# Performance work log

Hardware: AMD Instinct MI355X
Metric: run time of the kernel (lower is better)

Reference implementation:

```python
import jax, jax.numpy as jnp
import numpy as np

# Production-scale detection head dims
B_TOTAL = 16      # num_tbins(4) * batch_size(4)
NUM_ANCHORS = 100000
NUM_CLASSES = 8


def setup_inputs() -> dict:
    key = jax.random.key(0)
    k1, k2, k3, k4 = jax.random.split(key, 4)
    # anchors [A,4] = (cx, cy, w, h); widths/heights strictly positive
    ctr = jax.random.uniform(k1, (NUM_ANCHORS, 2), jnp.float32) * 512.0
    wh = jax.random.uniform(k2, (NUM_ANCHORS, 2), jnp.float32) * 64.0 + 8.0
    anchors = jnp.concatenate([ctr, wh], axis=-1)
    loc_preds = jax.random.normal(k3, (B_TOTAL, NUM_ANCHORS, 4), jnp.float32)
    # class scores in [0,1] (post-sigmoid semantics)
    cls_preds = jax.nn.sigmoid(jax.random.normal(k4, (B_TOTAL, NUM_ANCHORS, NUM_CLASSES), jnp.float32))
    return {
        "anchors": anchors,
        "loc_preds": loc_preds,
        "cls_preds": cls_preds,
        "varx": 0.1,
        "vary": 0.2,
        "score_thresh": 0.7,
        "batch_size": 4,
    }


def reference(anchors, loc_preds, cls_preds, varx, vary, score_thresh, batch_size):
    """Anchor decode + score-threshold filtering.

    Faithful to BoxDecoder.forward, but jit-compatible: instead of
    boolean-mask compaction into ragged per-(t,i) lists (data-dependent
    shapes), we return the dense [B*A*C, 6] box tensor plus the keep mask
    and batch_index; (mask, batch_index) fully determine the ragged
    targets[t][i] = box_tensor[mask & (batch_index == t*batch_size+i)].
    """
    B, A, C = cls_preds.shape
    # decode: xy = loc[:2]*varx*anchor_wh + anchor_xy ; wh = exp(loc[2:]*vary)*anchor_wh
    xy = loc_preds[..., :2] * varx * anchors[..., 2:] + anchors[..., :2]
    wh = jnp.exp(loc_preds[..., 2:] * vary) * anchors[..., 2:]
    box_preds = jnp.concatenate([xy - wh * 0.5, xy + wh * 0.5], axis=-1)  # [B,A,4]
    # expand boxes over classes, flatten to [B*A*C, ...] (same order as torch view(-1,...))
    boxes = jnp.broadcast_to(box_preds[:, :, None, :], (B, A, C, 4)).reshape(-1, 4)
    scores = cls_preds.reshape(-1)
    # idxs = b*C + c  ->  label = c+1, batch_index = b
    labels = jnp.broadcast_to(jnp.arange(C, dtype=jnp.float32) + 1.0, (B, A, C)).reshape(-1)
    batch_index = jnp.broadcast_to(jnp.arange(B, dtype=jnp.int32)[:, None, None], (B, A, C)).reshape(-1)
    box_tensor = jnp.concatenate([boxes, scores[:, None], labels[:, None]], axis=1)  # [B*A*C, 6]
    mask = scores >= score_thresh  # keep mask (compaction left to consumer / kernel)
    return box_tensor, mask, batch_index
```

## Files before the change

kernel.cpp:

```cpp
#include <hip/hip_runtime.h>
#include <math.h>


#define MAGIC_SHIFT 38

__global__ __launch_bounds__(256) void box_decode_kernel(
    const float4* __restrict__ anchors,
    const float4* __restrict__ loc,
    const float*  __restrict__ cls,
    const float*  __restrict__ varx_p,
    const float*  __restrict__ vary_p,
    const float*  __restrict__ th_p,
    float2*       __restrict__ out_box2,
    float*        __restrict__ out_mask,
    float*        __restrict__ out_bidx,
    unsigned n2,
    unsigned A, unsigned C,
    unsigned long long invA,
    unsigned long long invC)
{
    unsigned j = blockIdx.x * 256u + threadIdx.x;
    if (j >= n2) return;

    unsigned row = j / 3u;
    unsigned rem = j - row * 3u;

    unsigned t = (unsigned)(((unsigned long long)row * invC) >> MAGIC_SHIFT);
    unsigned c = row - t * C;
    unsigned b = (unsigned)(((unsigned long long)t * invA) >> MAGIC_SHIFT);
    unsigned a = t - b * A;

    float varx = *varx_p;
    float vary = *vary_p;
    float th   = *th_p;

    float4 anc = anchors[a];
    float4 lp  = loc[t];

    float x = fmaf(lp.x * varx, anc.z, anc.x);
    float y = fmaf(lp.y * varx, anc.w, anc.y);
    float w = expf(lp.z * vary) * anc.z;
    float h = expf(lp.w * vary) * anc.w;

    float score = cls[row];

    float2 r;
    if (rem == 0) {
        r.x = fmaf(w, -0.5f, x);
        r.y = fmaf(h, -0.5f, y);
    } else if (rem == 1) {
        r.x = fmaf(w, 0.5f, x);
        r.y = fmaf(h, 0.5f, y);
    } else {
        r.x = score;
        r.y = (float)(c + 1u);
    }
    out_box2[j] = r;

    if (rem == 2) {
        out_mask[row] = (score >= th) ? 1.0f : 0.0f;
        out_bidx[row] = (float)b;
    }
}

extern "C" void kernel_launch(void* const* d_in, const int* in_sizes, int n_in,
                              void* d_out, int out_size, void* d_ws, size_t ws_size,
                              hipStream_t stream) {
    const float* anchors = (const float*)d_in[0];
    const float* loc     = (const float*)d_in[1];
    const float* cls     = (const float*)d_in[2];
    const float* varx_p  = (const float*)d_in[3];
    const float* vary_p  = (const float*)d_in[4];
    const float* th_p    = (const float*)d_in[5];

    unsigned A = (unsigned)(in_sizes[0] / 4);
    unsigned B = (unsigned)((unsigned)in_sizes[1] / (4u * A));
    unsigned C = (unsigned)((unsigned)in_sizes[2] / (A * B));
    unsigned rows = B * A * C;
    unsigned n2 = rows * 3u;

    float* out_box  = (float*)d_out;
    float* out_mask = out_box + (size_t)rows * 6;
    float* out_bidx = out_mask + rows;

    unsigned long long invA = ((1ULL << MAGIC_SHIFT) / A) + 1ULL;
    unsigned long long invC = ((1ULL << MAGIC_SHIFT) / C) + 1ULL;

    dim3 grid((n2 + 255u) / 256u);
    box_decode_kernel<<<grid, dim3(256), 0, stream>>>(
        (const float4*)anchors, (const float4*)loc, cls,
        varx_p, vary_p, th_p,
        (float2*)out_box, out_mask, out_bidx,
        n2, A, C, invA, invC);
}
```

Baseline: 551.3 us.

## Widen box stores to float4 and split mask/bidx into separate blocks

Each thread now writes one float4 of the box tensor, with the 6-float rows grouped in pairs of classes so that three float4 stores cover two rows. The mask and batch-index outputs move to a dedicated tail range of blocks that read scores as float4 and write float4 results. This replaces the float2 stores and the scattered scalar mask/bidx writes from one thread in three, cutting store instructions and improving coalescing. In exchange the kernel assumes C is even and rows is divisible by 4, and each box thread still recomputes the exp-based decode.

```diff
diff --git a/kernel.cpp b/kernel.cpp
--- a/kernel.cpp
+++ b/kernel.cpp
@@ -11,55 +11,84 @@
     const float*  __restrict__ varx_p,
     const float*  __restrict__ vary_p,
     const float*  __restrict__ th_p,
-    float2*       __restrict__ out_box2,
-    float*        __restrict__ out_mask,
-    float*        __restrict__ out_bidx,
-    unsigned n2,
+    float4*       __restrict__ out_box4,
+    float4*       __restrict__ out_mask4,
+    float4*       __restrict__ out_bidx4,
+    unsigned n4,
+    unsigned nm4,
+    unsigned nb_box,
     unsigned A, unsigned C,
+    unsigned f4_per_t,
     unsigned long long invA,
-    unsigned long long invC)
+    unsigned long long invC,
+    unsigned long long invF)
 {
-    unsigned j = blockIdx.x * 256u + threadIdx.x;
-    if (j >= n2) return;
+    unsigned tid = threadIdx.x;
 
-    unsigned row = j / 3u;
-    unsigned rem = j - row * 3u;
+    if (blockIdx.x < nb_box) {
+        unsigned g = blockIdx.x * 256u + tid;
+        if (g >= n4) return;
 
-    unsigned t = (unsigned)(((unsigned long long)row * invC) >> MAGIC_SHIFT);
-    unsigned c = row - t * C;
-    unsigned b = (unsigned)(((unsigned long long)t * invA) >> MAGIC_SHIFT);
-    unsigned a = t - b * A;
+        unsigned t  = (unsigned)(((unsigned long long)g * invF) >> MAGIC_SHIFT);
+        unsigned j  = g - t * f4_per_t;
+        unsigned b  = (unsigned)(((unsigned long long)t * invA) >> MAGIC_SHIFT);
+        unsigned a  = t - b * A;
+        unsigned s  = j / 3u;
+        unsigned jm = j - s * 3u;
 
-    float varx = *varx_p;
-    float vary = *vary_p;
-    float th   = *th_p;
+        float varx = *varx_p;
+        float vary = *vary_p;
 
-    float4 anc = anchors[a];
-    float4 lp  = loc[t];
+        float4 anc = anchors[a];
+        float4 lp  = loc[t];
 
-    float x = fmaf(lp.x * varx, anc.z, anc.x);
-    float y = fmaf(lp.y * varx, anc.w, anc.y);
-    float w = expf(lp.z * vary) * anc.z;
-    float h = expf(lp.w * vary) * anc.w;
+        float x = fmaf(lp.x * varx, anc.z, anc.x);
+        float y = fmaf(lp.y * varx, anc.w, anc.y);
+        float w = expf(lp.z * vary) * anc.z;
+        float h = expf(lp.w * vary) * anc.w;
 
-    float score = cls[row];
+        float x1 = fmaf(w, -0.5f, x);
+        float y1 = fmaf(h, -0.5f, y);
+        float x2 = fmaf(w,  0.5f, x);
+        float y2 = fmaf(h,  0.5f, y);
 
-    float2 r;
-    if (rem == 0) {
-        r.x = fmaf(w, -0.5f, x);
-        r.y = fmaf(h, -0.5f, y);
-    } else if (rem == 1) {
-        r.x = fmaf(w, 0.5f, x);
-        r.y = fmaf(h, 0.5f, y);
+        unsigned r0 = t * C + 2u * s;
+
+        float4 r;
+        if (jm == 0u) {
+            r.x = x1; r.y = y1; r.z = x2; r.w = y2;
+        } else if (jm == 1u) {
+            r.x = cls[r0];
+            r.y = (float)(2u * s + 1u);
+            r.z = x1; r.w = y1;
+        } else {
+            r.x = x2; r.y = y2;
+            r.z = cls[r0 + 1u];
+            r.w = (float)(2u * s + 2u);
+        }
+        out_box4[g] = r;
     } else {
-        r.x = score;
-        r.y = (float)(c + 1u);
-    }
-    out_box2[j] = r;
+        unsigned k = (blockIdx.x - nb_box) * 256u + tid;
+        if (k >= nm4) return;
 
-    if (rem == 2) {
-        out_mask[row] = (score >= th) ? 1.0f : 0.0f;
-        out_bidx[row] = (float)b;
+        float th = *th_p;
+        const float4* cls4 = (const float4*)cls;
+        float4 sc = cls4[k];
+
+        unsigned row0 = k * 4u;
+        unsigned t2 = (unsigned)(((unsigned long long)row0 * invC) >> MAGIC_SHIFT);
+        unsigned b  = (unsigned)(((unsigned long long)t2  * invA) >> MAGIC_SHIFT);
+        float bf = (float)b;
+
+        float4 m;
+        m.x = (sc.x >= th) ? 1.0f : 0.0f;
+        m.y = (sc.y >= th) ? 1.0f : 0.0f;
+        m.z = (sc.z >= th) ? 1.0f : 0.0f;
+        m.w = (sc.w >= th) ? 1.0f : 0.0f;
+        out_mask4[k] = m;
+
+        float4 bv; bv.x = bf; bv.y = bf; bv.z = bf; bv.w = bf;
+        out_bidx4[k] = bv;
     }
 }
 
@@ -77,7 +106,10 @@
     unsigned B = (unsigned)((unsigned)in_sizes[1] / (4u * A));
     unsigned C = (unsigned)((unsigned)in_sizes[2] / (A * B));
     unsigned rows = B * A * C;
-    unsigned n2 = rows * 3u;
+
+    unsigned f4_per_t = (6u * C) / 4u;
+    unsigned n4  = rows * 6u / 4u;
+    unsigned nm4 = rows / 4u;
 
     float* out_box  = (float*)d_out;
     float* out_mask = out_box + (size_t)rows * 6;
@@ -85,11 +117,14 @@
 
     unsigned long long invA = ((1ULL << MAGIC_SHIFT) / A) + 1ULL;
     unsigned long long invC = ((1ULL << MAGIC_SHIFT) / C) + 1ULL;
+    unsigned long long invF = ((1ULL << MAGIC_SHIFT) / f4_per_t) + 1ULL;
 
-    dim3 grid((n2 + 255u) / 256u);
-    box_decode_kernel<<<grid, dim3(256), 0, stream>>>(
+    unsigned nb_box  = (n4  + 255u) / 256u;
+    unsigned nb_mask = (nm4 + 255u) / 256u;
+
+    box_decode_kernel<<<dim3(nb_box + nb_mask), dim3(256), 0, stream>>>(
         (const float4*)anchors, (const float4*)loc, cls,
         varx_p, vary_p, th_p,
-        (float2*)out_box, out_mask, out_bidx,
-        n2, A, C, invA, invC);
+        (float4*)out_box, (float4*)out_mask, (float4*)out_bidx,
+        n4, nm4, nb_box, A, C, f4_per_t, invA, invC, invF);
 }
```

Measured after the change: 523.2 us. 5.1% less time.
